# Performance work log

Hardware: AMD Instinct MI355X
Metric: run time of the kernel (lower is better)

The kernel has to match this reference:

```python
import jax, jax.numpy as jnp
import numpy as np

E, D, H, T = 8, 1024, 4096, 8192  # num_expert, d_model, d_hidden, total_tokens


def setup_inputs() -> dict:
    key = jax.random.key(0)
    k1, k2, k3, k4, k5 = jax.random.split(key, 5)
    inp = jax.random.normal(k1, (T, D), dtype=jnp.float32)
    # FMoELinear weights: [E, out_features, in_features], bias [E, out_features]
    w1 = jax.random.normal(k2, (E, H, D), dtype=jnp.float32) * 0.02
    b1 = jax.random.normal(k3, (E, H), dtype=jnp.float32) * 0.02
    w2 = jax.random.normal(k4, (E, D, H), dtype=jnp.float32) * 0.02
    b2 = jax.random.normal(k5, (E, D), dtype=jnp.float32) * 0.02
    # tokens are contiguous per expert; equal split here (counts may vary in general)
    fwd_expert_count = jnp.full((E,), T // E, dtype=jnp.int32)
    return {"inp": inp, "w1": w1, "b1": b1, "w2": w2, "b2": b2,
            "fwd_expert_count": fwd_expert_count}


def _expert_ids(counts, n_tokens):
    # token t belongs to expert e iff cumsum(counts)[e-1] <= t < cumsum(counts)[e]
    offsets = jnp.cumsum(counts)  # [E]
    t = jnp.arange(n_tokens)
    return jnp.sum(t[:, None] >= offsets[None, :], axis=1)  # [T] in [0, E]


def _grouped_linear(x, W, b, eid):
    # grouped GEMM: y[t] = W[eid[t]] @ x[t] + b[eid[t]]; tokens with eid >= E -> 0
    n_exp = W.shape[0]
    acc = jnp.zeros((x.shape[0], W.shape[1]), dtype=x.dtype)
    for e in range(n_exp):  # small fixed loop over experts
        ye = x @ W[e].T + b[e]
        acc = acc + jnp.where((eid == e)[:, None], ye, jnp.zeros((), x.dtype))
    return acc


def reference(inp, w1, b1, w2, b2, fwd_expert_count):
    eid = _expert_ids(fwd_expert_count, inp.shape[0])
    h = _grouped_linear(inp, w1, b1, eid)   # [T, H]
    h = jax.nn.gelu(h)
    out = _grouped_linear(h, w2, b2, eid)   # [T, D]
    return out
```

## Files before the change

### kernel.cpp

```cpp
#include <hip/hip_runtime.h>
#include <hip/hip_bf16.h>
#include <cstdint>
#include <cstddef>


using bf16 = __hip_bfloat16;
typedef __attribute__((ext_vector_type(8))) short bf16x8;
typedef __attribute__((ext_vector_type(4))) float f32x4;

#define BM 128
#define BN 128
#define BK 32

__device__ __forceinline__ float gelu_f(float x) {
  const float c0 = 0.7978845608028654f;
  const float c1 = 0.044715f;
  float u = c0 * (x + c1 * x * x * x);
  float t = 1.0f - 2.0f / (__expf(2.0f * u) + 1.0f);
  return 0.5f * x * (1.0f + t);
}

__device__ __forceinline__ void stage_f32(const float* g, bf16* lds,
                                          int srow, int seg, int ldg) {
#pragma unroll
  for (int h = 0; h < 2; ++h) {
    const float* p = g + (size_t)(srow + h * 64) * ldg + seg;
    f32x4 lo = *(const f32x4*)(p);
    f32x4 hi = *(const f32x4*)(p + 4);
    bf16 cv[8];
#pragma unroll
    for (int i = 0; i < 4; ++i) {
      cv[i]     = __float2bfloat16(lo[i]);
      cv[i + 4] = __float2bfloat16(hi[i]);
    }
    *(bf16x8*)&lds[(srow + h * 64) * BK + seg] = *(const bf16x8*)cv;
  }
}

__device__ __forceinline__ void stage_bf16(const bf16* g, bf16* lds,
                                           int srow, int seg, int ldg) {
#pragma unroll
  for (int h = 0; h < 2; ++h) {
    const bf16* p = g + (size_t)(srow + h * 64) * ldg + seg;
    *(bf16x8*)&lds[(srow + h * 64) * BK + seg] = *(const bf16x8*)p;
  }
}

template <bool AF32>
__global__ __launch_bounds__(256) void grouped_gemm_bt(
    const void* __restrict__ Av,
    const float* __restrict__ B,
    const float* __restrict__ bias,
    void* __restrict__ Cv,
    const int* __restrict__ counts,
    int E, int N, int K, int c_is_bf16_gelu)
{
  __shared__ alignas(16) bf16 As[BM * BK];
  __shared__ alignas(16) bf16 Bs[BN * BK];

  const int tid  = threadIdx.x;
  const int lane = tid & 63;
  const int wave = tid >> 6;
  const int m0 = blockIdx.y * BM;
  const int n0 = blockIdx.x * BN;

  int eid = 0;
  {
    long long cum = 0;
    for (int e = 0; e < E; ++e) { cum += counts[e]; if (m0 >= cum) eid = e + 1; }
  }

  const int wrow = (wave >> 1) * 64;
  const int wcol = (wave & 1) * 64;

  f32x4 acc[4][4] = {};

  if (eid < E) {
    const float* Bexp = B + (size_t)eid * (size_t)N * (size_t)K;
    const int srow = tid >> 2;
    const int seg  = (tid & 3) * 8;

    const int frow = lane & 15;
    const int fk   = (lane >> 4) * 8;

    for (int kt = 0; kt < K; kt += BK) {
      if (AF32)
        stage_f32((const float*)Av + (size_t)(m0 + srow) * K + kt - (size_t)srow * K,
                  As, srow, seg, K);
      else
        stage_bf16((const bf16*)Av + (size_t)(m0 + srow) * K + kt - (size_t)srow * K,
                   As, srow, seg, K);
      stage_f32(Bexp + (size_t)(n0 + srow) * K + kt - (size_t)srow * K,
                Bs, srow, seg, K);
      __syncthreads();

      bf16x8 af[4], bfr[4];
#pragma unroll
      for (int i = 0; i < 4; ++i)
        af[i] = *(const bf16x8*)&As[(wrow + i * 16 + frow) * BK + fk];
#pragma unroll
      for (int j = 0; j < 4; ++j)
        bfr[j] = *(const bf16x8*)&Bs[(wcol + j * 16 + frow) * BK + fk];

#pragma unroll
      for (int i = 0; i < 4; ++i)
#pragma unroll
        for (int j = 0; j < 4; ++j)
          acc[i][j] = __builtin_amdgcn_mfma_f32_16x16x32_bf16(af[i], bfr[j], acc[i][j], 0, 0, 0);

      __syncthreads();
    }
  }

  const int crow = (lane >> 4) * 4;
  const int ccol = lane & 15;
  const int do_gelu = c_is_bf16_gelu;

  if (eid < E) {
    float bv[4];
#pragma unroll
    for (int j = 0; j < 4; ++j)
      bv[j] = bias[(size_t)eid * N + n0 + wcol + j * 16 + ccol];
#pragma unroll
    for (int i = 0; i < 4; ++i) {
#pragma unroll
      for (int r = 0; r < 4; ++r) {
        size_t grow = (size_t)(m0 + wrow + i * 16 + crow + r);
#pragma unroll
        for (int j = 0; j < 4; ++j) {
          float v = acc[i][j][r] + bv[j];
          size_t idx = grow * N + n0 + wcol + j * 16 + ccol;
          if (do_gelu) ((bf16*)Cv)[idx] = __float2bfloat16(gelu_f(v));
          else         ((float*)Cv)[idx] = v;
        }
      }
    }
  } else {
#pragma unroll
    for (int i = 0; i < 4; ++i) {
#pragma unroll
      for (int r = 0; r < 4; ++r) {
        size_t grow = (size_t)(m0 + wrow + i * 16 + crow + r);
#pragma unroll
        for (int j = 0; j < 4; ++j) {
          size_t idx = grow * N + n0 + wcol + j * 16 + ccol;
          if (do_gelu) ((bf16*)Cv)[idx] = __float2bfloat16(0.0f);
          else         ((float*)Cv)[idx] = 0.0f;
        }
      }
    }
  }
}

extern "C" void kernel_launch(void* const* d_in, const int* in_sizes, int n_in,
                              void* d_out, int out_size, void* d_ws, size_t ws_size,
                              hipStream_t stream) {
  const float* inp = (const float*)d_in[0];
  const float* w1  = (const float*)d_in[1];
  const float* b1  = (const float*)d_in[2];
  const float* w2  = (const float*)d_in[3];
  const float* b2  = (const float*)d_in[4];
  const int* cnt   = (const int*)d_in[5];
  float* out = (float*)d_out;

  const int E = in_sizes[5];
  const int H = in_sizes[2] / E;
  const int D = in_sizes[4] / E;
  const int T = in_sizes[0] / D;

  bf16* h = (bf16*)d_ws;

  dim3 blk(256);
  dim3 g1(H / BN, T / BM);
  grouped_gemm_bt<true><<<g1, blk, 0, stream>>>(inp, w1, b1, h, cnt, E, H, D, 1);
  dim3 g2(D / BN, T / BM);
  grouped_gemm_bt<false><<<g2, blk, 0, stream>>>(h, w2, b2, out, cnt, E, D, H, 0);
}
```

Baseline: 554.9 us.

## Stage GEMM tiles via direct global-to-LDS loads with XOR-swizzled fp32 layout

```diff
diff --git a/kernel.cpp b/kernel.cpp
--- a/kernel.cpp
+++ b/kernel.cpp
@@ -11,6 +11,12 @@
 #define BM 128
 #define BN 128
 #define BK 32
+
+__device__ __forceinline__ void gll16(const void* g, void* l) {
+  __builtin_amdgcn_global_load_lds(
+      (const __attribute__((address_space(1))) void*)g,
+      (__attribute__((address_space(3))) void*)l, 16, 0, 0);
+}
 
 __device__ __forceinline__ float gelu_f(float x) {
   const float c0 = 0.7978845608028654f;
@@ -20,30 +26,14 @@
   return 0.5f * x * (1.0f + t);
 }
 
-__device__ __forceinline__ void stage_f32(const float* g, bf16* lds,
-                                          int srow, int seg, int ldg) {
-#pragma unroll
-  for (int h = 0; h < 2; ++h) {
-    const float* p = g + (size_t)(srow + h * 64) * ldg + seg;
-    f32x4 lo = *(const f32x4*)(p);
-    f32x4 hi = *(const f32x4*)(p + 4);
-    bf16 cv[8];
-#pragma unroll
-    for (int i = 0; i < 4; ++i) {
-      cv[i]     = __float2bfloat16(lo[i]);
-      cv[i + 4] = __float2bfloat16(hi[i]);
-    }
-    *(bf16x8*)&lds[(srow + h * 64) * BK + seg] = *(const bf16x8*)cv;
-  }
-}
-
-__device__ __forceinline__ void stage_bf16(const bf16* g, bf16* lds,
-                                           int srow, int seg, int ldg) {
-#pragma unroll
-  for (int h = 0; h < 2; ++h) {
-    const bf16* p = g + (size_t)(srow + h * 64) * ldg + seg;
-    *(bf16x8*)&lds[(srow + h * 64) * BK + seg] = *(const bf16x8*)p;
-  }
+__device__ __forceinline__ bf16x8 cvt8(f32x4 lo, f32x4 hi) {
+  bf16 cv[8];
+#pragma unroll
+  for (int q = 0; q < 4; ++q) {
+    cv[q]     = __float2bfloat16(lo[q]);
+    cv[q + 4] = __float2bfloat16(hi[q]);
+  }
+  return *(const bf16x8*)cv;
 }
 
 template <bool AF32>
@@ -55,8 +45,10 @@
     const int* __restrict__ counts,
     int E, int N, int K, int c_is_bf16_gelu)
 {
-  __shared__ alignas(16) bf16 As[BM * BK];
-  __shared__ alignas(16) bf16 Bs[BN * BK];
+  constexpr int ABYTES = AF32 ? (BM * BK * 4) : (BM * BK * 2);
+  __shared__ alignas(16) unsigned char smem[ABYTES + BN * BK * 4];
+  unsigned char* Asm = smem;
+  unsigned char* Bsm = smem + ABYTES;
 
   const int tid  = threadIdx.x;
   const int lane = tid & 63;
@@ -77,30 +69,68 @@
 
   if (eid < E) {
     const float* Bexp = B + (size_t)eid * (size_t)N * (size_t)K;
-    const int srow = tid >> 2;
-    const int seg  = (tid & 3) * 8;
+
+    const int srow8 = lane >> 3;
+    const int scol  = ((lane & 7) ^ srow8) * 4;
+    const float* gB = Bexp + (size_t)(n0 + wave * 32 + srow8) * K + scol;
+    unsigned char* lB = Bsm + (wave * 32) * 128;
+
+    const float* gAf = nullptr;
+    const bf16*  gAh = nullptr;
+    unsigned char* lA;
+    if constexpr (AF32) {
+      gAf = (const float*)Av + (size_t)(m0 + wave * 32 + srow8) * K + scol;
+      lA  = Asm + (wave * 32) * 128;
+    } else {
+      gAh = (const bf16*)Av + (size_t)(m0 + wave * 16 + (lane >> 2)) * K + (lane & 3) * 8;
+      lA  = Asm + (wave * 16) * 64;
+    }
 
     const int frow = lane & 15;
-    const int fk   = (lane >> 4) * 8;
+    const int s    = lane & 7;
+    const int cb   = (lane >> 4) * 2;
+    const unsigned char* rB_lo = Bsm + ((wcol + frow) * 8 + (cb ^ s)) * 16;
+    const unsigned char* rB_hi = Bsm + ((wcol + frow) * 8 + ((cb ^ 1) ^ s)) * 16;
+    const unsigned char* rA_lo;
+    const unsigned char* rA_hi = nullptr;
+    if constexpr (AF32) {
+      rA_lo = Asm + ((wrow + frow) * 8 + (cb ^ s)) * 16;
+      rA_hi = Asm + ((wrow + frow) * 8 + ((cb ^ 1) ^ s)) * 16;
+    } else {
+      rA_lo = Asm + ((wrow + frow) * BK + (lane >> 4) * 8) * 2;
+    }
 
     for (int kt = 0; kt < K; kt += BK) {
-      if (AF32)
-        stage_f32((const float*)Av + (size_t)(m0 + srow) * K + kt - (size_t)srow * K,
-                  As, srow, seg, K);
-      else
-        stage_bf16((const bf16*)Av + (size_t)(m0 + srow) * K + kt - (size_t)srow * K,
-                   As, srow, seg, K);
-      stage_f32(Bexp + (size_t)(n0 + srow) * K + kt - (size_t)srow * K,
-                Bs, srow, seg, K);
+#pragma unroll
+      for (int i = 0; i < 4; ++i)
+        gll16(gB + (size_t)i * 8 * K + kt, lB + i * 1024);
+      if constexpr (AF32) {
+#pragma unroll
+        for (int i = 0; i < 4; ++i)
+          gll16(gAf + (size_t)i * 8 * K + kt, lA + i * 1024);
+      } else {
+        gll16(gAh + kt, lA);
+        gll16(gAh + (size_t)64 * K + kt, lA + 4096);
+      }
       __syncthreads();
 
       bf16x8 af[4], bfr[4];
 #pragma unroll
-      for (int i = 0; i < 4; ++i)
-        af[i] = *(const bf16x8*)&As[(wrow + i * 16 + frow) * BK + fk];
-#pragma unroll
-      for (int j = 0; j < 4; ++j)
-        bfr[j] = *(const bf16x8*)&Bs[(wcol + j * 16 + frow) * BK + fk];
+      for (int i = 0; i < 4; ++i) {
+        if constexpr (AF32) {
+          f32x4 lo = *(const f32x4*)(rA_lo + i * 2048);
+          f32x4 hi = *(const f32x4*)(rA_hi + i * 2048);
+          af[i] = cvt8(lo, hi);
+        } else {
+          af[i] = *(const bf16x8*)(rA_lo + i * 1024);
+        }
+      }
+#pragma unroll
+      for (int j = 0; j < 4; ++j) {
+        f32x4 lo = *(const f32x4*)(rB_lo + j * 2048);
+        f32x4 hi = *(const f32x4*)(rB_hi + j * 2048);
+        bfr[j] = cvt8(lo, hi);
+      }
 
 #pragma unroll
       for (int i = 0; i < 4; ++i)
```

Result: slower. 617.3 us (+11.3%).
